# Optimization experiments

Hardware: AMD Instinct MI355X
Metric: run time of the kernel (lower is better)

Reference implementation:

```python
import jax, jax.numpy as jnp
import numpy as np


def setup_inputs() -> dict:
    key = jax.random.key(0)
    k1, k2 = jax.random.split(key)
    x = jax.random.normal(k1, (16, 2048, 512), dtype=jnp.float32)
    embed = jax.random.normal(k2, (4096, 512), dtype=jnp.float32)
    return {"x": x, "embed": embed}


def reference(x, embed):
    # encode: flatten leading dims, compute -||x - e||^2 via expansion, argmax
    shape = x.shape
    xf = x.reshape(-1, shape[-1])                       # [N, d]
    x_sq = jnp.sum(xf * xf, axis=1, keepdims=True)      # [N, 1]
    e_sq = jnp.sum(embed * embed, axis=1)[None, :]      # [1, K]
    dist = -(x_sq - 2.0 * (xf @ embed.T) + e_sq)        # [N, K]
    embed_ind = jnp.argmax(dist, axis=-1)               # [N]
    embed_ind = embed_ind.reshape(shape[:-1])           # [B, S]
    # decode: embedding lookup (dequantize)
    quantize = embed[embed_ind]                         # [B, S, d]
    return embed_ind, quantize
```

## Files before the change

### kernel.cpp

```cpp
#include <hip/hip_runtime.h>
#include <hip/hip_fp16.h>
#include <stdint.h>


typedef _Float16 f16;
typedef __attribute__((ext_vector_type(4))) _Float16 f16x4;
typedef __attribute__((ext_vector_type(8))) _Float16 f16x8;
typedef __attribute__((ext_vector_type(4))) float f32x4;

#define DDIM 512
#define KCODES 4096
#define NSPLIT 4
#define BM 128
#define BN 256
#define BK 32
#define PSTRIDE (NSPLIT * 2)

__device__ __forceinline__ void gload_lds16(const void* g, void* l) {
  __builtin_amdgcn_global_load_lds(
      (const __attribute__((address_space(1))) void*)g,
      (__attribute__((address_space(3))) void*)l,
      16, 0, 0);
}

__global__ void convert_split(const float* __restrict__ in,
                              f16* __restrict__ hi, f16* __restrict__ lo, int n4) {
  int stride = gridDim.x * blockDim.x;
  for (int i = blockIdx.x * blockDim.x + threadIdx.x; i < n4; i += stride) {
    float4 v = ((const float4*)in)[i];
    float vv[4] = {v.x, v.y, v.z, v.w};
    f16x4 h, l;
#pragma unroll
    for (int j = 0; j < 4; ++j) {
      _Float16 hh = (_Float16)vv[j];
      h[j] = hh;
      l[j] = (_Float16)(vv[j] - (float)hh);
    }
    ((f16x4*)hi)[i] = h;
    ((f16x4*)lo)[i] = l;
  }
}

__global__ void esq_kernel(const float* __restrict__ e, float* __restrict__ esq) {
  int gw = (blockIdx.x * blockDim.x + threadIdx.x) >> 6;
  int lane = threadIdx.x & 63;
  if (gw >= KCODES) return;
  const float4* row = (const float4*)(e + (size_t)gw * DDIM);
  float4 a = row[lane * 2];
  float4 b = row[lane * 2 + 1];
  double s = (double)a.x * a.x + (double)a.y * a.y + (double)a.z * a.z + (double)a.w * a.w +
             (double)b.x * b.x + (double)b.y * b.y + (double)b.z * b.z + (double)b.w * b.w;
#pragma unroll
  for (int m = 32; m; m >>= 1) s += __shfl_xor(s, m, 64);
  if (lane == 0) esq[gw] = (float)s;
}

__global__ __launch_bounds__(256, 2) void vq_main(
    const f16* __restrict__ Ah, const f16* __restrict__ Al,
    const f16* __restrict__ Bh, const f16* __restrict__ Bl,
    const float* __restrict__ esq, float2* __restrict__ partials, int nRowBlocks) {
  __shared__ f16 lds[24576];
  char* const AhB = (char*)lds;
  char* const AlB = AhB + 8192;
  char* const BhB = AhB + 16384;
  char* const BlB = AhB + 32768;

  int nwg = gridDim.x;
  int bid = blockIdx.x;
  int cpx = nwg >> 3;
  int swz = (bid & 7) * cpx + (bid >> 3);
  int nsp = swz / nRowBlocks;
  int brow = swz % nRowBlocks;
  int rowbase = brow * BM;

  int tid = threadIdx.x;
  int lane = tid & 63;
  int wv = tid >> 6;
  int wr = wv >> 1, wc = wv & 1;
  int l15 = lane & 15, lg = lane >> 4;

  const int aoff = (wr * 64 + l15) * 64 + lg * 16;
  const int boff = (wc * 128 + l15) * 64 + lg * 16;
  char* const stA = AhB + wv * 1024;
  char* const stB = BhB + wv * 1024;

  int srow = tid >> 2;
  int skoff = (tid & 3) * 8;

  float bestv[16];
  int besti[16];
#pragma unroll
  for (int t = 0; t < 16; ++t) { bestv[t] = -3.4e38f; besti[t] = 0; }

  const int codesPer = KCODES / NSPLIT;
  const f16* aSrcH = Ah + (size_t)(rowbase + srow) * DDIM + skoff;
  const f16* aSrcL = Al + (size_t)(rowbase + srow) * DDIM + skoff;

  for (int ch = 0; ch < codesPer / BN; ++ch) {
    int cbase = nsp * codesPer + ch * BN;
    const f16* bSrcH = Bh + (size_t)(cbase + srow) * DDIM + skoff;
    const f16* bSrcL = Bl + (size_t)(cbase + srow) * DDIM + skoff;

    f32x4 acc[4][8];
#pragma unroll
    for (int i = 0; i < 4; ++i)
#pragma unroll
      for (int j = 0; j < 8; ++j) acc[i][j] = (f32x4){0.f, 0.f, 0.f, 0.f};

#pragma unroll 1
    for (int kk = 0; kk < DDIM; kk += BK) {
      gload_lds16(aSrcH + kk, stA);
      gload_lds16(aSrcH + (size_t)64 * DDIM + kk, stA + 4096);
      gload_lds16(aSrcL + kk, stA + 8192);
      gload_lds16(aSrcL + (size_t)64 * DDIM + kk, stA + 8192 + 4096);
#pragma unroll
      for (int r = 0; r < 4; ++r) {
        gload_lds16(bSrcH + (size_t)(r * 64) * DDIM + kk, stB + r * 4096);
        gload_lds16(bSrcL + (size_t)(r * 64) * DDIM + kk, stB + 16384 + r * 4096);
      }
      __syncthreads();

      f16x8 ah[4], al[4], bh[8], bl[8];
#pragma unroll
      for (int i = 0; i < 4; ++i) ah[i] = *(const f16x8*)(AhB + aoff + i * 1024);
#pragma unroll
      for (int j = 0; j < 8; ++j) bh[j] = *(const f16x8*)(BhB + boff + j * 1024);
#pragma unroll
      for (int i = 0; i < 4; ++i)
#pragma unroll
        for (int j = 0; j < 8; ++j)
          acc[i][j] = __builtin_amdgcn_mfma_f32_16x16x32_f16(ah[i], bh[j], acc[i][j], 0, 0, 0);
#pragma unroll
      for (int i = 0; i < 4; ++i) al[i] = *(const f16x8*)(AlB + aoff + i * 1024);
#pragma unroll
      for (int i = 0; i < 4; ++i)
#pragma unroll
        for (int j = 0; j < 8; ++j)
          acc[i][j] = __builtin_amdgcn_mfma_f32_16x16x32_f16(al[i], bh[j], acc[i][j], 0, 0, 0);
#pragma unroll
      for (int j = 0; j < 8; ++j) bl[j] = *(const f16x8*)(BlB + boff + j * 1024);
#pragma unroll
      for (int i = 0; i < 4; ++i)
#pragma unroll
        for (int j = 0; j < 8; ++j)
          acc[i][j] = __builtin_amdgcn_mfma_f32_16x16x32_f16(ah[i], bl[j], acc[i][j], 0, 0, 0);
      __syncthreads();
    }

#pragma unroll
    for (int j = 0; j < 8; ++j) {
      int code = cbase + wc * 128 + j * 16 + l15;
      float eh = 0.5f * esq[code];
#pragma unroll
      for (int i = 0; i < 4; ++i)
#pragma unroll
        for (int r = 0; r < 4; ++r) {
          float v = acc[i][j][r] - eh;
          int t = i * 4 + r;
          if (v > bestv[t]) { bestv[t] = v; besti[t] = code; }
        }
    }
  }

#pragma unroll
  for (int m = 1; m < 16; m <<= 1) {
#pragma unroll
    for (int t = 0; t < 16; ++t) {
      float ov = __shfl_xor(bestv[t], m, 64);
      int oi = __shfl_xor(besti[t], m, 64);
      if (ov > bestv[t] || (ov == bestv[t] && oi < besti[t])) { bestv[t] = ov; besti[t] = oi; }
    }
  }
  if (l15 == 0) {
#pragma unroll
    for (int i = 0; i < 4; ++i)
#pragma unroll
      for (int r = 0; r < 4; ++r) {
        int row = rowbase + wr * 64 + i * 16 + lg * 4 + r;
        partials[(size_t)row * PSTRIDE + nsp * 2 + wc] =
            make_float2(bestv[i * 4 + r], (float)besti[i * 4 + r]);
      }
  }
}

__global__ void reduce_decode(const float* __restrict__ embed,
                              const float2* __restrict__ partials,
                              float* __restrict__ outIdx, float* __restrict__ outQ,
                              int nRows) {
  int gw = (blockIdx.x * blockDim.x + threadIdx.x) >> 6;
  int lane = threadIdx.x & 63;
  if (gw >= nRows) return;
  float bv = -3.4e38f;
  int bi = 0x7fffffff;
#pragma unroll
  for (int s = 0; s < PSTRIDE; ++s) {
    float2 p = partials[(size_t)gw * PSTRIDE + s];
    int idx = (int)p.y;
    if (p.x > bv || (p.x == bv && idx < bi)) { bv = p.x; bi = idx; }
  }
  if (lane == 0) outIdx[gw] = (float)bi;
  const float4* src = (const float4*)(embed + (size_t)bi * DDIM);
  float4* dst = (float4*)(outQ + (size_t)gw * DDIM);
  dst[lane] = src[lane];
  dst[lane + 64] = src[lane + 64];
}

extern "C" void kernel_launch(void* const* d_in, const int* in_sizes, int n_in,
                              void* d_out, int out_size, void* d_ws, size_t ws_size,
                              hipStream_t stream) {
  const float* x = (const float*)d_in[0];
  const float* embed = (const float*)d_in[1];
  int nX = in_sizes[0];
  int nRows = nX / DDIM;
  int nRowBlocks = nRows / BM;

  float* out = (float*)d_out;
  float* outIdx = out;
  float* outQ = out + nRows;

  size_t szA = (size_t)nRows * DDIM * sizeof(f16);
  size_t szB = (size_t)KCODES * DDIM * sizeof(f16);
  size_t szEsq = (size_t)KCODES * sizeof(float);
  size_t szPart = (size_t)nRows * PSTRIDE * sizeof(float2);

  char* ws = (char*)d_ws;
  f16 *Ah, *Al, *Bh, *Bl;
  float* esq;
  float2* parts;
  size_t needFull = 2 * szA + 2 * szB + szEsq + szPart;
  if (ws_size >= needFull) {
    Ah = (f16*)ws;
    Al = (f16*)(ws + szA);
    Bh = (f16*)(ws + 2 * szA);
    Bl = (f16*)(ws + 2 * szA + szB);
    esq = (float*)(ws + 2 * szA + 2 * szB);
    parts = (float2*)(ws + 2 * szA + 2 * szB + szEsq);
  } else {
    Ah = (f16*)outQ;
    Al = Ah + (size_t)nRows * DDIM;
    Bh = (f16*)ws;
    Bl = (f16*)(ws + szB);
    esq = (float*)(ws + 2 * szB);
    parts = (float2*)(ws + 2 * szB + szEsq);
  }

  int n4x = nX / 4;
  int n4e = in_sizes[1] / 4;
  hipLaunchKernelGGL(convert_split, dim3(2048), dim3(256), 0, stream, x, Ah, Al, n4x);
  hipLaunchKernelGGL(convert_split, dim3((n4e + 255) / 256), dim3(256), 0, stream, embed, Bh, Bl, n4e);
  hipLaunchKernelGGL(esq_kernel, dim3(KCODES / 4), dim3(256), 0, stream, embed, esq);
  hipLaunchKernelGGL(vq_main, dim3(nRowBlocks * NSPLIT), dim3(256), 0, stream,
                     Ah, Al, Bh, Bl, esq, parts, nRowBlocks);
  hipLaunchKernelGGL(reduce_decode, dim3(nRows / 4), dim3(256), 0, stream,
                     embed, parts, outIdx, outQ, nRows);
}
```

Measured before the change: 416.9 us.

## Double-buffer LDS staging with 256x256 tiles and 512-thread blocks

```diff
diff --git a/kernel.cpp b/kernel.cpp
--- a/kernel.cpp
+++ b/kernel.cpp
@@ -10,10 +10,12 @@
 
 #define DDIM 512
 #define KCODES 4096
-#define NSPLIT 4
-#define BM 128
+#define NSPLIT 2
+#define BM 256
 #define BN 256
 #define BK 32
+#define NCH ((KCODES / NSPLIT) / BN)
+#define NSTEPS (NCH * (DDIM / BK))
 #define PSTRIDE (NSPLIT * 2)
 
 __device__ __forceinline__ void gload_lds16(const void* g, void* l) {
@@ -55,15 +57,11 @@
   if (lane == 0) esq[gw] = (float)s;
 }
 
-__global__ __launch_bounds__(256, 2) void vq_main(
+__global__ __launch_bounds__(512, 2) void vq_main(
     const f16* __restrict__ Ah, const f16* __restrict__ Al,
     const f16* __restrict__ Bh, const f16* __restrict__ Bl,
     const float* __restrict__ esq, float2* __restrict__ partials, int nRowBlocks) {
-  __shared__ f16 lds[24576];
-  char* const AhB = (char*)lds;
-  char* const AlB = AhB + 8192;
-  char* const BhB = AhB + 16384;
-  char* const BlB = AhB + 32768;
+  __shared__ char lds[131072];
 
   int nwg = gridDim.x;
   int bid = blockIdx.x;
@@ -81,85 +79,97 @@
 
   const int aoff = (wr * 64 + l15) * 64 + lg * 16;
   const int boff = (wc * 128 + l15) * 64 + lg * 16;
-  char* const stA = AhB + wv * 1024;
-  char* const stB = BhB + wv * 1024;
 
   int srow = tid >> 2;
   int skoff = (tid & 3) * 8;
+  const int codesPer = KCODES / NSPLIT;
+
+  const f16* aSrcH = Ah + (size_t)(rowbase + srow) * DDIM + skoff;
+  const f16* aSrcL = Al + (size_t)(rowbase + srow) * DDIM + skoff;
+  const f16* bBaseH = Bh + (size_t)(nsp * codesPer + srow) * DDIM + skoff;
+  const f16* bBaseL = Bl + (size_t)(nsp * codesPer + srow) * DDIM + skoff;
+
+  auto STAGE = [&](int buf, int ch, int kk) {
+    char* base = lds + buf * 65536 + wv * 1024;
+    size_t bo = (size_t)(ch * BN) * DDIM + kk;
+    gload_lds16(aSrcH + kk, base);
+    gload_lds16(aSrcH + kk + (size_t)128 * DDIM, base + 8192);
+    gload_lds16(aSrcL + kk, base + 16384);
+    gload_lds16(aSrcL + kk + (size_t)128 * DDIM, base + 16384 + 8192);
+    gload_lds16(bBaseH + bo, base + 32768);
+    gload_lds16(bBaseH + bo + (size_t)128 * DDIM, base + 32768 + 8192);
+    gload_lds16(bBaseL + bo, base + 49152);
+    gload_lds16(bBaseL + bo + (size_t)128 * DDIM, base + 49152 + 8192);
+  };
 
   float bestv[16];
   int besti[16];
 #pragma unroll
   for (int t = 0; t < 16; ++t) { bestv[t] = -3.4e38f; besti[t] = 0; }
 
-  const int codesPer = KCODES / NSPLIT;
-  const f16* aSrcH = Ah + (size_t)(rowbase + srow) * DDIM + skoff;
-  const f16* aSrcL = Al + (size_t)(rowbase + srow) * DDIM + skoff;
-
-  for (int ch = 0; ch < codesPer / BN; ++ch) {
-    int cbase = nsp * codesPer + ch * BN;
-    const f16* bSrcH = Bh + (size_t)(cbase + srow) * DDIM + skoff;
-    const f16* bSrcL = Bl + (size_t)(cbase + srow) * DDIM + skoff;
-
-    f32x4 acc[4][8];
-#pragma unroll
-    for (int i = 0; i < 4; ++i)
-#pragma unroll
-      for (int j = 0; j < 8; ++j) acc[i][j] = (f32x4){0.f, 0.f, 0.f, 0.f};
-
+  f32x4 acc[4][8];
+
+  STAGE(0, 0, 0);
+  __syncthreads();
+
+  int buf = 0;
 #pragma unroll 1
-    for (int kk = 0; kk < DDIM; kk += BK) {
-      gload_lds16(aSrcH + kk, stA);
-      gload_lds16(aSrcH + (size_t)64 * DDIM + kk, stA + 4096);
-      gload_lds16(aSrcL + kk, stA + 8192);
-      gload_lds16(aSrcL + (size_t)64 * DDIM + kk, stA + 8192 + 4096);
-#pragma unroll
-      for (int r = 0; r < 4; ++r) {
-        gload_lds16(bSrcH + (size_t)(r * 64) * DDIM + kk, stB + r * 4096);
-        gload_lds16(bSrcL + (size_t)(r * 64) * DDIM + kk, stB + 16384 + r * 4096);
+  for (int s = 0; s < NSTEPS; ++s) {
+    int ch = s >> 4;
+    int ns = s + 1;
+    if (ns < NSTEPS) STAGE(buf ^ 1, ns >> 4, (ns & 15) * BK);
+
+    if ((s & 15) == 0) {
+#pragma unroll
+      for (int i = 0; i < 4; ++i)
+#pragma unroll
+        for (int j = 0; j < 8; ++j) acc[i][j] = (f32x4){0.f, 0.f, 0.f, 0.f};
+    }
+
+    char* base = lds + buf * 65536;
+    f16x8 ah[4], al[4], bh[8], bl[8];
+#pragma unroll
+    for (int i = 0; i < 4; ++i) ah[i] = *(const f16x8*)(base + aoff + i * 1024);
+#pragma unroll
+    for (int j = 0; j < 8; ++j) bh[j] = *(const f16x8*)(base + 32768 + boff + j * 1024);
+#pragma unroll
+    for (int i = 0; i < 4; ++i)
+#pragma unroll
+      for (int j = 0; j < 8; ++j)
+        acc[i][j] = __builtin_amdgcn_mfma_f32_16x16x32_f16(ah[i], bh[j], acc[i][j], 0, 0, 0);
+#pragma unroll
+    for (int i = 0; i < 4; ++i) al[i] = *(const f16x8*)(base + 16384 + aoff + i * 1024);
+#pragma unroll
+    for (int i = 0; i < 4; ++i)
+#pragma unroll
+      for (int j = 0; j < 8; ++j)
+        acc[i][j] = __builtin_amdgcn_mfma_f32_16x16x32_f16(al[i], bh[j], acc[i][j], 0, 0, 0);
+#pragma unroll
+    for (int j = 0; j < 8; ++j) bl[j] = *(const f16x8*)(base + 49152 + boff + j * 1024);
+#pragma unroll
+    for (int i = 0; i < 4; ++i)
+#pragma unroll
+      for (int j = 0; j < 8; ++j)
+        acc[i][j] = __builtin_amdgcn_mfma_f32_16x16x32_f16(ah[i], bl[j], acc[i][j], 0, 0, 0);
+
+    if ((s & 15) == 15) {
+      int cbase = nsp * codesPer + ch * BN;
+#pragma unroll
+      for (int j = 0; j < 8; ++j) {
+        int code = cbase + wc * 128 + j * 16 + l15;
+        float eh = 0.5f * esq[code];
+#pragma unroll
+        for (int i = 0; i < 4; ++i)
+#pragma unroll
+          for (int r = 0; r < 4; ++r) {
+            float v = acc[i][j][r] - eh;
+            int t = i * 4 + r;
+            if (v > bestv[t]) { bestv[t] = v; besti[t] = code; }
+          }
       }
-      __syncthreads();
-
-      f16x8 ah[4], al[4], bh[8], bl[8];
-#pragma unroll
-      for (int i = 0; i < 4; ++i) ah[i] = *(const f16x8*)(AhB + aoff + i * 1024);
-#pragma unroll
-      for (int j = 0; j < 8; ++j) bh[j] = *(const f16x8*)(BhB + boff + j * 1024);
-#pragma unroll
-      for (int i = 0; i < 4; ++i)
-#pragma unroll
-        for (int j = 0; j < 8; ++j)
-          acc[i][j] = __builtin_amdgcn_mfma_f32_16x16x32_f16(ah[i], bh[j], acc[i][j], 0, 0, 0);
-#pragma unroll
-      for (int i = 0; i < 4; ++i) al[i] = *(const f16x8*)(AlB + aoff + i * 1024);
-#pragma unroll
-      for (int i = 0; i < 4; ++i)
-#pragma unroll
-        for (int j = 0; j < 8; ++j)
-          acc[i][j] = __builtin_amdgcn_mfma_f32_16x16x32_f16(al[i], bh[j], acc[i][j], 0, 0, 0);
-#pragma unroll
-      for (int j = 0; j < 8; ++j) bl[j] = *(const f16x8*)(BlB + boff + j * 1024);
-#pragma unroll
-      for (int i = 0; i < 4; ++i)
-#pragma unroll
-        for (int j = 0; j < 8; ++j)
-          acc[i][j] = __builtin_amdgcn_mfma_f32_16x16x32_f16(ah[i], bl[j], acc[i][j], 0, 0, 0);
-      __syncthreads();
-    }
-
-#pragma unroll
-    for (int j = 0; j < 8; ++j) {
-      int code = cbase + wc * 128 + j * 16 + l15;
-      float eh = 0.5f * esq[code];
-#pragma unroll
-      for (int i = 0; i < 4; ++i)
-#pragma unroll
-        for (int r = 0; r < 4; ++r) {
-          float v = acc[i][j][r] - eh;
-          int t = i * 4 + r;
-          if (v > bestv[t]) { bestv[t] = v; besti[t] = code; }
-        }
-    }
+    }
+    __syncthreads();
+    buf ^= 1;
   }
 
 #pragma unroll
@@ -249,7 +259,7 @@
   hipLaunchKernelGGL(convert_split, dim3(2048), dim3(256), 0, stream, x, Ah, Al, n4x);
   hipLaunchKernelGGL(convert_split, dim3((n4e + 255) / 256), dim3(256), 0, stream, embed, Bh, Bl, n4e);
   hipLaunchKernelGGL(esq_kernel, dim3(KCODES / 4), dim3(256), 0, stream, embed, esq);
-  hipLaunchKernelGGL(vq_main, dim3(nRowBlocks * NSPLIT), dim3(256), 0, stream,
+  hipLaunchKernelGGL(vq_main, dim3(nRowBlocks * NSPLIT), dim3(512), 0, stream,
                      Ah, Al, Bh, Bl, esq, parts, nRowBlocks);
   hipLaunchKernelGGL(reduce_decode, dim3(nRows / 4), dim3(256), 0, stream,
                      embed, parts, outIdx, outQ, nRows);
```

New measurement: 379.4 us. -9.0%, faster.
